# Kernel optimization log

Hardware: AMD Instinct MI355X
Metric: run time of the kernel (lower is better)

## Reference

```python
import jax, jax.numpy as jnp
import numpy as np

B, C, N = 16, 32, 131072


def setup_inputs() -> dict:
    key = jax.random.key(0)
    k1, k2 = jax.random.split(key)
    pred = jax.random.normal(k1, (B, C, N), dtype=jnp.float32)
    true = jax.random.randint(k2, (B, N), 0, C, dtype=jnp.int32)
    return {"pred": pred, "true": true}


def reference(pred, true):
    """FPCELossV3.

    Torch loop semantics: for class i, pos_i are the point indices n (over ALL
    batch rows, with multiplicity) where true[b', n] == i; the term
    -log(p)/p at pred[b, i, n] is summed over every batch b and every such
    occurrence. Equivalent to weighting f(pred[b, i, n]) by
    count[i, n] = sum_{b'} [true[b', n] == i].
    """
    Bc, Cc, Nc = pred.shape
    logp = jax.nn.log_softmax(pred, axis=1)          # (B,C,N)
    p = jnp.exp(logp)
    f = -logp / p                                    # -log(p)/p, (B,C,N)
    # count[c, n] = number of batch rows b' with true[b', n] == c
    counts = jnp.sum(jax.nn.one_hot(true, Cc, dtype=pred.dtype), axis=0).T  # (C,N)
    loss = jnp.sum(f * counts[None, :, :]) / Nc
    return loss
```

## Files before the change

kernel.cpp:

```cpp
#include <hip/hip_runtime.h>


#define B_TOT   16
#define C_CLS   32
#define BSPLIT  8
#define TPB     256

__global__ __launch_bounds__(TPB) void fpce_partial(
    const float* __restrict__ pred, const int* __restrict__ tru,
    float* __restrict__ partial, int N) {
  const int half = blockIdx.x & 1;
  const int nblk = blockIdx.x >> 1;
  const int n    = nblk * TPB + threadIdx.x;
  const int b0   = half * BSPLIT;

  int t[B_TOT];
#pragma unroll
  for (int j = 0; j < B_TOT; ++j) t[j] = tru[(size_t)j * N + n];

  float S[BSPLIT], T0[BSPLIT], T1[BSPLIT];
#pragma unroll
  for (int j = 0; j < BSPLIT; ++j) { S[j] = 0.f; T0[j] = 0.f; T1[j] = 0.f; }

  const float* p0 = pred + (size_t)b0 * C_CLS * N + n;

  for (int c = 0; c < C_CLS; ++c) {
    float x[BSPLIT];
#pragma unroll
    for (int j = 0; j < BSPLIT; ++j)
      x[j] = p0[(size_t)(j * C_CLS + c) * N];

    int cnt = 0;
#pragma unroll
    for (int j = 0; j < B_TOT; ++j) cnt += (t[j] == c);
    const float cf = (float)cnt;

#pragma unroll
    for (int j = 0; j < BSPLIT; ++j) {
      const float e = __expf(x[j]);
      S[j] += e;
      const float r = __expf(-x[j]);
      const float u = cf * r;
      T0[j] += u;
      T1[j] = fmaf(u, x[j], T1[j]);
    }
  }

  float W = 0.f;
#pragma unroll
  for (int j = 0; j < BSPLIT; ++j) {
    const float L = __logf(S[j]);
    W += S[j] * (L * T0[j] - T1[j]);
  }

#pragma unroll
  for (int off = 32; off > 0; off >>= 1) W += __shfl_down(W, off, 64);

  __shared__ float swave[TPB / 64];
  const int lane = threadIdx.x & 63;
  const int wid  = threadIdx.x >> 6;
  if (lane == 0) swave[wid] = W;
  __syncthreads();
  if (threadIdx.x == 0)
    partial[blockIdx.x] = swave[0] + swave[1] + swave[2] + swave[3];
}

__global__ __launch_bounds__(TPB) void fpce_final(
    const float* __restrict__ partial, float* __restrict__ out,
    int nblocks, float invN) {
  float v = 0.f;
  for (int i = threadIdx.x; i < nblocks; i += TPB) v += partial[i];
#pragma unroll
  for (int off = 32; off > 0; off >>= 1) v += __shfl_down(v, off, 64);
  __shared__ float sw[TPB / 64];
  const int lane = threadIdx.x & 63;
  const int wid  = threadIdx.x >> 6;
  if (lane == 0) sw[wid] = v;
  __syncthreads();
  if (threadIdx.x == 0)
    out[0] = (sw[0] + sw[1] + sw[2] + sw[3]) * invN;
}

extern "C" void kernel_launch(void* const* d_in, const int* in_sizes, int n_in,
                              void* d_out, int out_size, void* d_ws, size_t ws_size,
                              hipStream_t stream) {
  const float* pred = (const float*)d_in[0];
  const int*   tru  = (const int*)d_in[1];
  float*       out  = (float*)d_out;
  float*       part = (float*)d_ws;

  const int N    = in_sizes[1] / B_TOT;
  const int nblk = (N / TPB) * (B_TOT / BSPLIT);

  fpce_partial<<<nblk, TPB, 0, stream>>>(pred, tru, part, N);
  fpce_final<<<1, TPB, 0, stream>>>(part, out, nblk, 1.0f / (float)N);
}
```

Before: 364.8 us.

## Process all batches per thread and replace final reduction kernel with atomics

Each thread now handles all 16 batch rows instead of half, so the labels are read once per point instead of twice. The second reduction kernel is dropped in favour of a per-wavefront atomicAdd into a zeroed output, and the class loop is unrolled by four. This cuts one launch and the duplicated label reads, but doubles per-thread registers (16 rows of S/T0/T1 plus loads), halves the grid size and makes the float sum order nondeterministic.

```diff
diff --git a/kernel.cpp b/kernel.cpp
--- a/kernel.cpp
+++ b/kernel.cpp
@@ -1,33 +1,30 @@
 #include <hip/hip_runtime.h>
 
 
-#define B_TOT   16
-#define C_CLS   32
-#define BSPLIT  8
-#define TPB     256
+#define B_TOT 16
+#define C_CLS 32
+#define TPB   256
 
-__global__ __launch_bounds__(TPB) void fpce_partial(
+__global__ __launch_bounds__(TPB) void fpce_kernel(
     const float* __restrict__ pred, const int* __restrict__ tru,
-    float* __restrict__ partial, int N) {
-  const int half = blockIdx.x & 1;
-  const int nblk = blockIdx.x >> 1;
-  const int n    = nblk * TPB + threadIdx.x;
-  const int b0   = half * BSPLIT;
+    float* __restrict__ out, int N, float invN) {
+  const int n = blockIdx.x * TPB + threadIdx.x;
 
   int t[B_TOT];
 #pragma unroll
   for (int j = 0; j < B_TOT; ++j) t[j] = tru[(size_t)j * N + n];
 
-  float S[BSPLIT], T0[BSPLIT], T1[BSPLIT];
+  float S[B_TOT], T0[B_TOT], T1[B_TOT];
 #pragma unroll
-  for (int j = 0; j < BSPLIT; ++j) { S[j] = 0.f; T0[j] = 0.f; T1[j] = 0.f; }
+  for (int j = 0; j < B_TOT; ++j) { S[j] = 0.f; T0[j] = 0.f; T1[j] = 0.f; }
 
-  const float* p0 = pred + (size_t)b0 * C_CLS * N + n;
+  const float* p0 = pred + n;
 
+#pragma unroll 4
   for (int c = 0; c < C_CLS; ++c) {
-    float x[BSPLIT];
+    float x[B_TOT];
 #pragma unroll
-    for (int j = 0; j < BSPLIT; ++j)
+    for (int j = 0; j < B_TOT; ++j)
       x[j] = p0[(size_t)(j * C_CLS + c) * N];
 
     int cnt = 0;
@@ -36,11 +33,9 @@
     const float cf = (float)cnt;
 
 #pragma unroll
-    for (int j = 0; j < BSPLIT; ++j) {
-      const float e = __expf(x[j]);
-      S[j] += e;
-      const float r = __expf(-x[j]);
-      const float u = cf * r;
+    for (int j = 0; j < B_TOT; ++j) {
+      S[j] += __expf(x[j]);
+      const float u = cf * __expf(-x[j]);
       T0[j] += u;
       T1[j] = fmaf(u, x[j], T1[j]);
     }
@@ -48,37 +43,15 @@
 
   float W = 0.f;
 #pragma unroll
-  for (int j = 0; j < BSPLIT; ++j) {
+  for (int j = 0; j < B_TOT; ++j) {
     const float L = __logf(S[j]);
     W += S[j] * (L * T0[j] - T1[j]);
   }
+  W *= invN;
 
 #pragma unroll
   for (int off = 32; off > 0; off >>= 1) W += __shfl_down(W, off, 64);
-
-  __shared__ float swave[TPB / 64];
-  const int lane = threadIdx.x & 63;
-  const int wid  = threadIdx.x >> 6;
-  if (lane == 0) swave[wid] = W;
-  __syncthreads();
-  if (threadIdx.x == 0)
-    partial[blockIdx.x] = swave[0] + swave[1] + swave[2] + swave[3];
-}
-
-__global__ __launch_bounds__(TPB) void fpce_final(
-    const float* __restrict__ partial, float* __restrict__ out,
-    int nblocks, float invN) {
-  float v = 0.f;
-  for (int i = threadIdx.x; i < nblocks; i += TPB) v += partial[i];
-#pragma unroll
-  for (int off = 32; off > 0; off >>= 1) v += __shfl_down(v, off, 64);
-  __shared__ float sw[TPB / 64];
-  const int lane = threadIdx.x & 63;
-  const int wid  = threadIdx.x >> 6;
-  if (lane == 0) sw[wid] = v;
-  __syncthreads();
-  if (threadIdx.x == 0)
-    out[0] = (sw[0] + sw[1] + sw[2] + sw[3]) * invN;
+  if ((threadIdx.x & 63) == 0) atomicAdd(out, W);
 }
 
 extern "C" void kernel_launch(void* const* d_in, const int* in_sizes, int n_in,
@@ -87,11 +60,9 @@
   const float* pred = (const float*)d_in[0];
   const int*   tru  = (const int*)d_in[1];
   float*       out  = (float*)d_out;
-  float*       part = (float*)d_ws;
 
-  const int N    = in_sizes[1] / B_TOT;
-  const int nblk = (N / TPB) * (B_TOT / BSPLIT);
+  const int N = in_sizes[1] / B_TOT;
 
-  fpce_partial<<<nblk, TPB, 0, stream>>>(pred, tru, part, N);
-  fpce_final<<<1, TPB, 0, stream>>>(part, out, nblk, 1.0f / (float)N);
+  hipMemsetAsync(out, 0, sizeof(float), stream);
+  fpce_kernel<<<N / TPB, TPB, 0, stream>>>(pred, tru, out, N, 1.0f / (float)N);
 }
```

Result: slower. 373.7 us (+2.5%).
